# Optimization experiments

Hardware: AMD Instinct MI355X
Metric: run time of the kernel (lower is better)

## Reference

```python
import jax, jax.numpy as jnp
import numpy as np

N_NODES = 100000
N_EDGES = 3200000
IN_FEATS = 512
HIDDEN = 16
OUT_FEATS = 128
N_CLASSES = 3


def _glorot(key, shape):
    fan_in, fan_out = shape[0], shape[1]
    limit = float(np.sqrt(6.0 / (fan_in + fan_out)))
    return jax.random.uniform(key, shape, jnp.float32, -limit, limit)


def setup_inputs() -> dict:
    key = jax.random.key(0)
    ks = jax.random.split(key, 9)
    features = jax.random.normal(ks[0], (N_NODES, IN_FEATS), jnp.float32)
    src = jax.random.randint(ks[1], (N_EDGES,), 0, N_NODES, jnp.int64)
    dst = jax.random.randint(ks[2], (N_EDGES,), 0, N_NODES, jnp.int64)
    W1 = _glorot(ks[3], (IN_FEATS, HIDDEN))
    b1 = jnp.zeros((HIDDEN,), jnp.float32)
    W2 = _glorot(ks[4], (HIDDEN, OUT_FEATS))
    b2 = jnp.zeros((OUT_FEATS,), jnp.float32)
    lim = float(1.0 / np.sqrt(OUT_FEATS))
    Wfc = jax.random.uniform(ks[5], (OUT_FEATS, N_CLASSES), jnp.float32, -lim, lim)
    bfc = jax.random.uniform(ks[6], (N_CLASSES,), jnp.float32, -lim, lim)
    return {"features": features, "src": src, "dst": dst,
            "W1": W1, "b1": b1, "W2": W2, "b2": b2, "Wfc": Wfc, "bfc": bfc}


def _graph_conv(feat, src, dst, W, b):
    # DGL GraphConv, norm='both': D_out^{-1/2} A D_in^{-1/2} feat W + b
    ones = jnp.ones((src.shape[0],), feat.dtype)
    deg_out = jax.ops.segment_sum(ones, src, num_segments=N_NODES)
    deg_in = jax.ops.segment_sum(ones, dst, num_segments=N_NODES)
    norm_src = jax.lax.rsqrt(jnp.maximum(deg_out, 1.0))  # [N]
    norm_dst = jax.lax.rsqrt(jnp.maximum(deg_in, 1.0))   # [N]
    # project first (in >= out here), then aggregate over edges
    h = (feat * norm_src[:, None]) @ W                   # [N, out]
    agg = jax.ops.segment_sum(h[src], dst, num_segments=N_NODES)  # [N, out]
    return agg * norm_dst[:, None] + b


def reference(features, src, dst, W1, b1, W2, b2, Wfc, bfc):
    x = jax.nn.relu(_graph_conv(features, src, dst, W1, b1))
    x = _graph_conv(x, src, dst, W2, b2)
    return x @ Wfc + bfc
```

## Files before the change

### kernel.cpp

```cpp
#include <hip/hip_runtime.h>

#define N_NODES 100000
#define N_EDGES 3200000
#define F_IN 512
#define NH 16
#define F_OUT 128
#define NCLS 3

#define NB 782
#define BCAP 4736
#define CHUNK 4096

typedef float  f32x4 __attribute__((ext_vector_type(4)));
typedef short  s16x8 __attribute__((ext_vector_type(8)));

static __device__ __forceinline__ short f2bf(float f) {
    union { float f; unsigned u; } v; v.f = f;
    unsigned r = v.u + 0x7FFFu + ((v.u >> 16) & 1u);
    return (short)(r >> 16);
}

__global__ __launch_bounds__(256) void bin_scatter_kernel(const int* __restrict__ src,
                                                          const int* __restrict__ dst,
                                                          int* __restrict__ deg_out,
                                                          int* __restrict__ gcursor,
                                                          int* __restrict__ pairbuf) {
    __shared__ int hist[NB];
    __shared__ int base[NB];
    int t = threadIdx.x;
    for (int i = t; i < NB; i += 256) hist[i] = 0;
    __syncthreads();
    int e0 = blockIdx.x * CHUNK;
    int nE = N_EDGES - e0; if (nE > CHUNK) nE = CHUNK;
    int pk[16], bk[16], rk[16];
#pragma unroll
    for (int it = 0; it < 16; ++it) {
        int i = t + it * 256;
        bool valid = i < nE;
        int s = valid ? src[e0 + i] : 0;
        int d = valid ? dst[e0 + i] : 0;
        if (valid) atomicAdd(&deg_out[s], 1);
        int b = d >> 7;
        pk[it] = s | ((d & 127) << 17);
        bk[it] = b;
        rk[it] = valid ? atomicAdd(&hist[b], 1) : 0;
    }
    __syncthreads();
    int rot = blockIdx.x % NB;
    for (int j = t; j < NB; j += 256) {
        int b = j + rot; if (b >= NB) b -= NB;
        int h = hist[b];
        base[b] = (h > 0) ? atomicAdd(&gcursor[b], h) : 0;
    }
    __syncthreads();
#pragma unroll
    for (int it = 0; it < 16; ++it) {
        int i = t + it * 256;
        if (i < nE) {
            int b = bk[it];
            int pos = base[b] + rk[it];
            if (pos < BCAP) pairbuf[b * BCAP + pos] = pk[it];
        }
    }
}

__global__ __launch_bounds__(1024) void bucket_scan_kernel(const int* __restrict__ gcursor,
                                                           int* __restrict__ csr_base) {
    __shared__ int s[1024];
    int t = threadIdx.x;
    int v = 0;
    if (t < NB) { v = gcursor[t]; if (v > BCAP) v = BCAP; }
    s[t] = v;
    __syncthreads();
    for (int off = 1; off < 1024; off <<= 1) {
        int x = (t >= off) ? s[t - off] : 0;
        __syncthreads();
        s[t] += x;
        __syncthreads();
    }
    if (t < NB) csr_base[t] = s[t] - v;
}

__global__ __launch_bounds__(256) void bucket_csr_kernel(const int* __restrict__ gcursor,
                                                         const int* __restrict__ csr_base,
                                                         const int* __restrict__ pairbuf,
                                                         int* __restrict__ col,
                                                         int* __restrict__ row_ptr,
                                                         float* __restrict__ norm_dst) {
    __shared__ int hist[128];
    __shared__ int scn[128];
    int b = blockIdx.x;
    int t = threadIdx.x;
    if (t < 128) hist[t] = 0;
    __syncthreads();
    int c = gcursor[b]; if (c > BCAP) c = BCAP;
    const int* pb = pairbuf + b * BCAP;
    int pk[19], rk[19];
#pragma unroll
    for (int it = 0; it < 19; ++it) {
        int i = t + it * 256;
        bool valid = i < c;
        int v = valid ? pb[i] : 0;
        pk[it] = v;
        rk[it] = valid ? atomicAdd(&hist[v >> 17], 1) : 0;
    }
    __syncthreads();
    if (t < 128) scn[t] = hist[t];
    __syncthreads();
    for (int off = 1; off < 128; off <<= 1) {
        int x = (t >= off && t < 128) ? scn[t - off] : 0;
        __syncthreads();
        if (t < 128) scn[t] += x;
        __syncthreads();
    }
    int gbase = csr_base[b];
#pragma unroll
    for (int it = 0; it < 19; ++it) {
        int i = t + it * 256;
        if (i < c) {
            int v = pk[it];
            int node = v >> 17;
            int pos = gbase + (scn[node] - hist[node]) + rk[it];
            col[pos] = v & 0x1FFFF;
        }
    }
    int node = b * 128 + t;
    if (t < 128 && node < N_NODES) {
        row_ptr[node] = gbase + scn[t] - hist[t];
        norm_dst[node] = rsqrtf(fmaxf((float)hist[t], 1.0f));
    }
    if (b == NB - 1 && t == 0) row_ptr[N_NODES] = N_EDGES;
}

__global__ void norm_src_kernel(const int* __restrict__ deg_out, float* __restrict__ norm_src) {
    int i = blockIdx.x * blockDim.x + threadIdx.x;
    if (i < N_NODES) norm_src[i] = rsqrtf(fmaxf((float)deg_out[i], 1.0f));
}

__global__ void w1b_prep_kernel(const float* __restrict__ W1, unsigned short* __restrict__ W1B) {
    int idx = blockIdx.x * blockDim.x + threadIdx.x;
    if (idx >= 16 * 64 * 8) return;
    int kc = idx >> 9, lane = (idx >> 3) & 63, i = idx & 7;
    int k = kc * 32 + (lane >> 4) * 8 + i;
    int j = lane & 15;
    W1B[idx] = (unsigned short)f2bf(W1[k * NH + j]);
}

__global__ void wc_prep_kernel(const float* __restrict__ W2, const float* __restrict__ b2,
                               const float* __restrict__ Wfc, const float* __restrict__ bfc,
                               float* __restrict__ Wc) {
    int t = threadIdx.x;
    if (t < NH * NCLS) {
        int j = t / NCLS, c = t % NCLS;
        float acc = 0.0f;
        for (int k = 0; k < F_OUT; ++k) acc += W2[j * F_OUT + k] * Wfc[k * NCLS + c];
        Wc[t] = acc;
    } else if (t < NH * NCLS + NCLS) {
        int c = t - NH * NCLS;
        float acc = bfc[c];
        for (int k = 0; k < F_OUT; ++k) acc += b2[k] * Wfc[k * NCLS + c];
        Wc[t] = acc;
    }
}

__global__ __launch_bounds__(256) void gemm1_kernel(const float* __restrict__ feat,
                                                    const unsigned short* __restrict__ W1B,
                                                    const float* __restrict__ norm_src,
                                                    float* __restrict__ h1) {
    int t = threadIdx.x;
    int lane = t & 63;
    int m = lane & 15;
    int q = lane >> 4;
    const s16x8* wb = (const s16x8*)W1B;
    s16x8 B[16];
#pragma unroll
    for (int kc = 0; kc < 16; ++kc) B[kc] = wb[kc * 64 + lane];

    int w = blockIdx.x * 4 + (t >> 6);
    int nwaves = gridDim.x * 4;
    const int ntiles = N_NODES / 16;
    for (int tile = w; tile < ntiles; tile += nwaves) {
        f32x4 acc = {0.0f, 0.0f, 0.0f, 0.0f};
        const float* arow = feat + (size_t)(tile * 16 + m) * F_IN + q * 8;
#pragma unroll
        for (int kc = 0; kc < 16; ++kc) {
            f32x4 fa = *(const f32x4*)(arow + kc * 32);
            f32x4 fb = *(const f32x4*)(arow + kc * 32 + 4);
            s16x8 a;
            a[0] = f2bf(fa.x); a[1] = f2bf(fa.y); a[2] = f2bf(fa.z); a[3] = f2bf(fa.w);
            a[4] = f2bf(fb.x); a[5] = f2bf(fb.y); a[6] = f2bf(fb.z); a[7] = f2bf(fb.w);
            acc = __builtin_amdgcn_mfma_f32_16x16x32_bf16(a, B[kc], acc, 0, 0, 0);
        }
#pragma unroll
        for (int r = 0; r < 4; ++r) {
            int node = tile * 16 + q * 4 + r;
            h1[(size_t)node * NH + m] = acc[r] * norm_src[node];
        }
    }
}

__global__ __launch_bounds__(256) void agg1_kernel(const int* __restrict__ row_ptr,
                                                   const int* __restrict__ col,
                                                   const float* __restrict__ h1,
                                                   const float* __restrict__ norm_dst,
                                                   const float* __restrict__ norm_src,
                                                   const float* __restrict__ b1,
                                                   float* __restrict__ x1n) {
    int t = threadIdx.x;
    int lane = t & 63;
    int n = blockIdx.x * 4 + (t >> 6);
    int eo = lane >> 2, comp = lane & 3;
    int beg = row_ptr[n], end = row_ptr[n + 1];
    f32x4 acc = {0.0f, 0.0f, 0.0f, 0.0f};
    for (int e = beg + eo; e < end; e += 16) {
        int s = col[e];
        acc += *(const f32x4*)(h1 + (size_t)s * NH + comp * 4);
    }
#pragma unroll
    for (int sh = 4; sh <= 32; sh <<= 1) {
        acc.x += __shfl_xor(acc.x, sh); acc.y += __shfl_xor(acc.y, sh);
        acc.z += __shfl_xor(acc.z, sh); acc.w += __shfl_xor(acc.w, sh);
    }
    if (lane < 4) {
        float nd = norm_dst[n], ns = norm_src[n];
        f32x4 bv = ((const f32x4*)b1)[lane];
        f32x4 v = acc * nd + bv;
        v.x = fmaxf(v.x, 0.0f) * ns; v.y = fmaxf(v.y, 0.0f) * ns;
        v.z = fmaxf(v.z, 0.0f) * ns; v.w = fmaxf(v.w, 0.0f) * ns;
        ((f32x4*)(x1n + (size_t)n * NH))[lane] = v;
    }
}

__global__ __launch_bounds__(256) void agg2_kernel(const int* __restrict__ row_ptr,
                                                   const int* __restrict__ col,
                                                   const float* __restrict__ x1n,
                                                   const float* __restrict__ norm_dst,
                                                   const float* __restrict__ Wc,
                                                   float* __restrict__ out) {
    __shared__ float Wcs[NH * NCLS + NCLS];
    int t = threadIdx.x;
    if (t < NH * NCLS + NCLS) Wcs[t] = Wc[t];
    __syncthreads();
    int lane = t & 63;
    int n = blockIdx.x * 4 + (t >> 6);
    int eo = lane >> 2, comp = lane & 3;
    int beg = row_ptr[n], end = row_ptr[n + 1];
    f32x4 acc = {0.0f, 0.0f, 0.0f, 0.0f};
    for (int e = beg + eo; e < end; e += 16) {
        int s = col[e];
        acc += *(const f32x4*)(x1n + (size_t)s * NH + comp * 4);
    }
#pragma unroll
    for (int sh = 4; sh <= 32; sh <<= 1) {
        acc.x += __shfl_xor(acc.x, sh); acc.y += __shfl_xor(acc.y, sh);
        acc.z += __shfl_xor(acc.z, sh); acc.w += __shfl_xor(acc.w, sh);
    }
    float p0 = 0.0f, p1 = 0.0f, p2 = 0.0f;
    if (lane < 4) {
#pragma unroll
        for (int i = 0; i < 4; ++i) {
            float y = acc[i];
            int j = lane * 4 + i;
            p0 += y * Wcs[j * NCLS + 0];
            p1 += y * Wcs[j * NCLS + 1];
            p2 += y * Wcs[j * NCLS + 2];
        }
    }
    p0 += __shfl_xor(p0, 1); p0 += __shfl_xor(p0, 2);
    p1 += __shfl_xor(p1, 1); p1 += __shfl_xor(p1, 2);
    p2 += __shfl_xor(p2, 1); p2 += __shfl_xor(p2, 2);
    if (lane == 0) {
        float nd = norm_dst[n];
        out[(size_t)n * NCLS + 0] = nd * p0 + Wcs[NH * NCLS + 0];
        out[(size_t)n * NCLS + 1] = nd * p1 + Wcs[NH * NCLS + 1];
        out[(size_t)n * NCLS + 2] = nd * p2 + Wcs[NH * NCLS + 2];
    }
}

extern "C" void kernel_launch(void* const* d_in, const int* in_sizes, int n_in,
                              void* d_out, int out_size, void* d_ws, size_t ws_size,
                              hipStream_t stream) {
    const float* feat = (const float*)d_in[0];
    const int*   src  = (const int*)d_in[1];
    const int*   dst  = (const int*)d_in[2];
    const float* W1   = (const float*)d_in[3];
    const float* b1   = (const float*)d_in[4];
    const float* W2   = (const float*)d_in[5];
    const float* b2   = (const float*)d_in[6];
    const float* Wfc  = (const float*)d_in[7];
    const float* bfc  = (const float*)d_in[8];
    float* out = (float*)d_out;

    char* ws = (char*)d_ws;
    size_t off = 0;
    auto carve = [&](size_t bytes) {
        char* p = ws + off;
        off = (off + bytes + 255) & ~(size_t)255;
        return p;
    };
    int*   deg_out  = (int*)carve((size_t)N_NODES * 4);
    int*   gcursor  = (int*)carve((size_t)NB * 4);
    int*   csr_base = (int*)carve((size_t)NB * 4);
    int*   pairbuf  = (int*)carve((size_t)NB * BCAP * 4);
    int*   row_ptr  = (int*)carve((size_t)(N_NODES + 1) * 4);
    int*   col      = (int*)carve((size_t)N_EDGES * 4);
    float* norm_src = (float*)carve((size_t)N_NODES * 4);
    float* norm_dst = (float*)carve((size_t)N_NODES * 4);
    float* h1       = (float*)carve((size_t)N_NODES * NH * 4);
    float* x1n      = (float*)carve((size_t)N_NODES * NH * 4);
    unsigned short* W1B = (unsigned short*)carve(16 * 64 * 8 * 2);
    float* Wc       = (float*)carve((NH * NCLS + NCLS) * 4);
    (void)ws_size;

    hipMemsetAsync(deg_out, 0, (size_t)N_NODES * 4, stream);
    hipMemsetAsync(gcursor, 0, (size_t)NB * 4, stream);

    const int nBinBlocks = (N_EDGES + CHUNK - 1) / CHUNK;
    bin_scatter_kernel<<<nBinBlocks, 256, 0, stream>>>(src, dst, deg_out, gcursor, pairbuf);
    bucket_scan_kernel<<<1, 1024, 0, stream>>>(gcursor, csr_base);
    bucket_csr_kernel<<<NB, 256, 0, stream>>>(gcursor, csr_base, pairbuf, col, row_ptr, norm_dst);

    norm_src_kernel<<<(N_NODES + 255) / 256, 256, 0, stream>>>(deg_out, norm_src);

    w1b_prep_kernel<<<32, 256, 0, stream>>>(W1, W1B);
    wc_prep_kernel<<<1, 64, 0, stream>>>(W2, b2, Wfc, bfc, Wc);

    gemm1_kernel<<<625, 256, 0, stream>>>(feat, W1B, norm_src, h1);

    agg1_kernel<<<N_NODES / 4, 256, 0, stream>>>(row_ptr, col, h1, norm_dst, norm_src, b1, x1n);

    agg2_kernel<<<N_NODES / 4, 256, 0, stream>>>(row_ptr, col, x1n, norm_dst, Wc, out);
}
```

Baseline: 599.8 us.

## Replace CSR build with bucketed edge lists aggregated via LDS atomics

Removes the scan and per-bucket CSR construction kernels and aggregates each layer directly from 256-node destination buckets. Each bucket block accumulates neighbor features into shared memory with float atomics and counts in-degree on the fly, so the norm_src and norm_dst arrays and kernels go away. This drops several launches and the col/row_ptr memory traffic. In exchange it pays for heavy LDS atomic contention, makes float summation order nondeterministic, and silently drops edges if a bucket overflows its capacity.

```diff
diff --git a/kernel.cpp b/kernel.cpp
--- a/kernel.cpp
+++ b/kernel.cpp
@@ -7,9 +7,9 @@
 #define F_OUT 128
 #define NCLS 3
 
-#define NB 782
-#define BCAP 4736
-#define CHUNK 4096
+#define NB 391
+#define BCAP 9216
+#define CHUNK 16384
 
 typedef float  f32x4 __attribute__((ext_vector_type(4)));
 typedef short  s16x8 __attribute__((ext_vector_type(8)));
@@ -20,121 +20,38 @@
     return (short)(r >> 16);
 }
 
-__global__ __launch_bounds__(256) void bin_scatter_kernel(const int* __restrict__ src,
-                                                          const int* __restrict__ dst,
-                                                          int* __restrict__ deg_out,
-                                                          int* __restrict__ gcursor,
-                                                          int* __restrict__ pairbuf) {
+__global__ __launch_bounds__(512) void bin_kernel(const int* __restrict__ src,
+                                                  const int* __restrict__ dst,
+                                                  int* __restrict__ deg_out,
+                                                  int* __restrict__ gcursor,
+                                                  int* __restrict__ pairbuf) {
     __shared__ int hist[NB];
-    __shared__ int base[NB];
+    __shared__ int cur[NB];
     int t = threadIdx.x;
-    for (int i = t; i < NB; i += 256) hist[i] = 0;
+    for (int i = t; i < NB; i += 512) hist[i] = 0;
     __syncthreads();
     int e0 = blockIdx.x * CHUNK;
     int nE = N_EDGES - e0; if (nE > CHUNK) nE = CHUNK;
-    int pk[16], bk[16], rk[16];
-#pragma unroll
-    for (int it = 0; it < 16; ++it) {
-        int i = t + it * 256;
-        bool valid = i < nE;
-        int s = valid ? src[e0 + i] : 0;
-        int d = valid ? dst[e0 + i] : 0;
-        if (valid) atomicAdd(&deg_out[s], 1);
-        int b = d >> 7;
-        pk[it] = s | ((d & 127) << 17);
-        bk[it] = b;
-        rk[it] = valid ? atomicAdd(&hist[b], 1) : 0;
+    for (int i = t; i < nE; i += 512) {
+        int d = dst[e0 + i];
+        atomicAdd(&hist[d >> 8], 1);
     }
     __syncthreads();
     int rot = blockIdx.x % NB;
-    for (int j = t; j < NB; j += 256) {
+    for (int j = t; j < NB; j += 512) {
         int b = j + rot; if (b >= NB) b -= NB;
         int h = hist[b];
-        base[b] = (h > 0) ? atomicAdd(&gcursor[b], h) : 0;
-    }
-    __syncthreads();
-#pragma unroll
-    for (int it = 0; it < 16; ++it) {
-        int i = t + it * 256;
-        if (i < nE) {
-            int b = bk[it];
-            int pos = base[b] + rk[it];
-            if (pos < BCAP) pairbuf[b * BCAP + pos] = pk[it];
-        }
-    }
-}
-
-__global__ __launch_bounds__(1024) void bucket_scan_kernel(const int* __restrict__ gcursor,
-                                                           int* __restrict__ csr_base) {
-    __shared__ int s[1024];
-    int t = threadIdx.x;
-    int v = 0;
-    if (t < NB) { v = gcursor[t]; if (v > BCAP) v = BCAP; }
-    s[t] = v;
-    __syncthreads();
-    for (int off = 1; off < 1024; off <<= 1) {
-        int x = (t >= off) ? s[t - off] : 0;
-        __syncthreads();
-        s[t] += x;
-        __syncthreads();
-    }
-    if (t < NB) csr_base[t] = s[t] - v;
-}
-
-__global__ __launch_bounds__(256) void bucket_csr_kernel(const int* __restrict__ gcursor,
-                                                         const int* __restrict__ csr_base,
-                                                         const int* __restrict__ pairbuf,
-                                                         int* __restrict__ col,
-                                                         int* __restrict__ row_ptr,
-                                                         float* __restrict__ norm_dst) {
-    __shared__ int hist[128];
-    __shared__ int scn[128];
-    int b = blockIdx.x;
-    int t = threadIdx.x;
-    if (t < 128) hist[t] = 0;
-    __syncthreads();
-    int c = gcursor[b]; if (c > BCAP) c = BCAP;
-    const int* pb = pairbuf + b * BCAP;
-    int pk[19], rk[19];
-#pragma unroll
-    for (int it = 0; it < 19; ++it) {
-        int i = t + it * 256;
-        bool valid = i < c;
-        int v = valid ? pb[i] : 0;
-        pk[it] = v;
-        rk[it] = valid ? atomicAdd(&hist[v >> 17], 1) : 0;
-    }
-    __syncthreads();
-    if (t < 128) scn[t] = hist[t];
-    __syncthreads();
-    for (int off = 1; off < 128; off <<= 1) {
-        int x = (t >= off && t < 128) ? scn[t - off] : 0;
-        __syncthreads();
-        if (t < 128) scn[t] += x;
-        __syncthreads();
-    }
-    int gbase = csr_base[b];
-#pragma unroll
-    for (int it = 0; it < 19; ++it) {
-        int i = t + it * 256;
-        if (i < c) {
-            int v = pk[it];
-            int node = v >> 17;
-            int pos = gbase + (scn[node] - hist[node]) + rk[it];
-            col[pos] = v & 0x1FFFF;
-        }
-    }
-    int node = b * 128 + t;
-    if (t < 128 && node < N_NODES) {
-        row_ptr[node] = gbase + scn[t] - hist[t];
-        norm_dst[node] = rsqrtf(fmaxf((float)hist[t], 1.0f));
-    }
-    if (b == NB - 1 && t == 0) row_ptr[N_NODES] = N_EDGES;
-}
-
-__global__ void norm_src_kernel(const int* __restrict__ deg_out, float* __restrict__ norm_src) {
-    int i = blockIdx.x * blockDim.x + threadIdx.x;
-    if (i < N_NODES) norm_src[i] = rsqrtf(fmaxf((float)deg_out[i], 1.0f));
+        cur[b] = (h > 0) ? atomicAdd(&gcursor[b], h) : 0;
+    }
+    __syncthreads();
+    for (int i = t; i < nE; i += 512) {
+        int s = src[e0 + i];
+        int d = dst[e0 + i];
+        atomicAdd(&deg_out[s], 1);
+        int b = d >> 8;
+        int pos = atomicAdd(&cur[b], 1);
+        if (pos < BCAP) pairbuf[b * BCAP + pos] = s | ((d & 255) << 17);
+    }
 }
 
 __global__ void w1b_prep_kernel(const float* __restrict__ W1, unsigned short* __restrict__ W1B) {
@@ -165,7 +82,7 @@
 
 __global__ __launch_bounds__(256) void gemm1_kernel(const float* __restrict__ feat,
                                                     const unsigned short* __restrict__ W1B,
-                                                    const float* __restrict__ norm_src,
+                                                    const int* __restrict__ deg_out,
                                                     float* __restrict__ h1) {
     int t = threadIdx.x;
     int lane = t & 63;
@@ -194,86 +111,110 @@
 #pragma unroll
         for (int r = 0; r < 4; ++r) {
             int node = tile * 16 + q * 4 + r;
-            h1[(size_t)node * NH + m] = acc[r] * norm_src[node];
-        }
-    }
-}
-
-__global__ __launch_bounds__(256) void agg1_kernel(const int* __restrict__ row_ptr,
-                                                   const int* __restrict__ col,
-                                                   const float* __restrict__ h1,
-                                                   const float* __restrict__ norm_dst,
-                                                   const float* __restrict__ norm_src,
-                                                   const float* __restrict__ b1,
-                                                   float* __restrict__ x1n) {
-    int t = threadIdx.x;
-    int lane = t & 63;
-    int n = blockIdx.x * 4 + (t >> 6);
+            float ns = rsqrtf(fmaxf((float)deg_out[node], 1.0f));
+            h1[(size_t)node * NH + m] = acc[r] * ns;
+        }
+    }
+}
+
+__global__ __launch_bounds__(512) void agg1_bucket_kernel(const int* __restrict__ gcursor,
+                                                          const int* __restrict__ pairbuf,
+                                                          const float* __restrict__ h1,
+                                                          const int* __restrict__ deg_out,
+                                                          const float* __restrict__ b1,
+                                                          float* __restrict__ x1n) {
+    __shared__ float acc[256 * 17];
+    __shared__ int   cnt[256];
+    __shared__ float b1s[16];
+    int b = blockIdx.x, t = threadIdx.x;
+    for (int i = t; i < 256 * 17; i += 512) acc[i] = 0.0f;
+    if (t < 256) cnt[t] = 0;
+    if (t < 16) b1s[t] = b1[t];
+    __syncthreads();
+    int c = gcursor[b]; if (c > BCAP) c = BCAP;
+    const int* pb = pairbuf + (size_t)b * BCAP;
+    int lane = t & 63, w = t >> 6;
     int eo = lane >> 2, comp = lane & 3;
-    int beg = row_ptr[n], end = row_ptr[n + 1];
-    f32x4 acc = {0.0f, 0.0f, 0.0f, 0.0f};
-    for (int e = beg + eo; e < end; e += 16) {
-        int s = col[e];
-        acc += *(const f32x4*)(h1 + (size_t)s * NH + comp * 4);
-    }
-#pragma unroll
-    for (int sh = 4; sh <= 32; sh <<= 1) {
-        acc.x += __shfl_xor(acc.x, sh); acc.y += __shfl_xor(acc.y, sh);
-        acc.z += __shfl_xor(acc.z, sh); acc.w += __shfl_xor(acc.w, sh);
-    }
-    if (lane < 4) {
-        float nd = norm_dst[n], ns = norm_src[n];
-        f32x4 bv = ((const f32x4*)b1)[lane];
-        f32x4 v = acc * nd + bv;
-        v.x = fmaxf(v.x, 0.0f) * ns; v.y = fmaxf(v.y, 0.0f) * ns;
-        v.z = fmaxf(v.z, 0.0f) * ns; v.w = fmaxf(v.w, 0.0f) * ns;
-        ((f32x4*)(x1n + (size_t)n * NH))[lane] = v;
-    }
-}
-
-__global__ __launch_bounds__(256) void agg2_kernel(const int* __restrict__ row_ptr,
-                                                   const int* __restrict__ col,
-                                                   const float* __restrict__ x1n,
-                                                   const float* __restrict__ norm_dst,
-                                                   const float* __restrict__ Wc,
-                                                   float* __restrict__ out) {
+    for (int e0 = w * 16; e0 < c; e0 += 128) {
+        int e = e0 + eo;
+        if (e < c) {
+            int pk = pb[e];
+            int s = pk & 0x1FFFF;
+            int loc = pk >> 17;
+            f32x4 hv = *(const f32x4*)(h1 + (size_t)s * NH + comp * 4);
+            int base = loc * 17 + comp * 4;
+            atomicAdd(&acc[base + 0], hv.x);
+            atomicAdd(&acc[base + 1], hv.y);
+            atomicAdd(&acc[base + 2], hv.z);
+            atomicAdd(&acc[base + 3], hv.w);
+            if (comp == 0) atomicAdd(&cnt[loc], 1);
+        }
+    }
+    __syncthreads();
+    int node = b * 256 + t;
+    if (t < 256 && node < N_NODES) {
+        float nd = rsqrtf(fmaxf((float)cnt[t], 1.0f));
+        float ns = rsqrtf(fmaxf((float)deg_out[node], 1.0f));
+        f32x4* dstp = (f32x4*)(x1n + (size_t)node * NH);
+#pragma unroll
+        for (int g = 0; g < 4; ++g) {
+            f32x4 v;
+            v.x = fmaxf(acc[t * 17 + g * 4 + 0] * nd + b1s[g * 4 + 0], 0.0f) * ns;
+            v.y = fmaxf(acc[t * 17 + g * 4 + 1] * nd + b1s[g * 4 + 1], 0.0f) * ns;
+            v.z = fmaxf(acc[t * 17 + g * 4 + 2] * nd + b1s[g * 4 + 2], 0.0f) * ns;
+            v.w = fmaxf(acc[t * 17 + g * 4 + 3] * nd + b1s[g * 4 + 3], 0.0f) * ns;
+            dstp[g] = v;
+        }
+    }
+}
+
+__global__ __launch_bounds__(512) void agg2_bucket_kernel(const int* __restrict__ gcursor,
+                                                          const int* __restrict__ pairbuf,
+                                                          const float* __restrict__ x1n,
+                                                          const float* __restrict__ Wc,
+                                                          float* __restrict__ out) {
+    __shared__ float acc[256 * 17];
+    __shared__ int   cnt[256];
     __shared__ float Wcs[NH * NCLS + NCLS];
-    int t = threadIdx.x;
+    int b = blockIdx.x, t = threadIdx.x;
+    for (int i = t; i < 256 * 17; i += 512) acc[i] = 0.0f;
+    if (t < 256) cnt[t] = 0;
     if (t < NH * NCLS + NCLS) Wcs[t] = Wc[t];
     __syncthreads();
-    int lane = t & 63;
-    int n = blockIdx.x * 4 + (t >> 6);
+    int c = gcursor[b]; if (c > BCAP) c = BCAP;
+    const int* pb = pairbuf + (size_t)b * BCAP;
+    int lane = t & 63, w = t >> 6;
     int eo = lane >> 2, comp = lane & 3;
-    int beg = row_ptr[n], end = row_ptr[n + 1];
-    f32x4 acc = {0.0f, 0.0f, 0.0f, 0.0f};
-    for (int e = beg + eo; e < end; e += 16) {
-        int s = col[e];
-        acc += *(const f32x4*)(x1n + (size_t)s * NH + comp * 4);
-    }
-#pragma unroll
-    for (int sh = 4; sh <= 32; sh <<= 1) {
-        acc.x += __shfl_xor(acc.x, sh); acc.y += __shfl_xor(acc.y, sh);
-        acc.z += __shfl_xor(acc.z, sh); acc.w += __shfl_xor(acc.w, sh);
-    }
-    float p0 = 0.0f, p1 = 0.0f, p2 = 0.0f;
-    if (lane < 4) {
-#pragma unroll
-        for (int i = 0; i < 4; ++i) {
-            float y = acc[i];
-            int j = lane * 4 + i;
+    for (int e0 = w * 16; e0 < c; e0 += 128) {
+        int e = e0 + eo;
+        if (e < c) {
+            int pk = pb[e];
+            int s = pk & 0x1FFFF;
+            int loc = pk >> 17;
+            f32x4 hv = *(const f32x4*)(x1n + (size_t)s * NH + comp * 4);
+            int base = loc * 17 + comp * 4;
+            atomicAdd(&acc[base + 0], hv.x);
+            atomicAdd(&acc[base + 1], hv.y);
+            atomicAdd(&acc[base + 2], hv.z);
+            atomicAdd(&acc[base + 3], hv.w);
+            if (comp == 0) atomicAdd(&cnt[loc], 1);
+        }
+    }
+    __syncthreads();
+    int node = b * 256 + t;
+    if (t < 256 && node < N_NODES) {
+        float nd = rsqrtf(fmaxf((float)cnt[t], 1.0f));
+        float p0 = 0.0f, p1 = 0.0f, p2 = 0.0f;
+#pragma unroll
+        for (int j = 0; j < NH; ++j) {
+            float y = acc[t * 17 + j];
             p0 += y * Wcs[j * NCLS + 0];
             p1 += y * Wcs[j * NCLS + 1];
             p2 += y * Wcs[j * NCLS + 2];
         }
-    }
-    p0 += __shfl_xor(p0, 1); p0 += __shfl_xor(p0, 2);
-    p1 += __shfl_xor(p1, 1); p1 += __shfl_xor(p1, 2);
-    p2 += __shfl_xor(p2, 1); p2 += __shfl_xor(p2, 2);
-    if (lane == 0) {
-        float nd = norm_dst[n];
-        out[(size_t)n * NCLS + 0] = nd * p0 + Wcs[NH * NCLS + 0];
-        out[(size_t)n * NCLS + 1] = nd * p1 + Wcs[NH * NCLS + 1];
-        out[(size_t)n * NCLS + 2] = nd * p2 + Wcs[NH * NCLS + 2];
+        out[(size_t)node * NCLS + 0] = nd * p0 + Wcs[NH * NCLS + 0];
+        out[(size_t)node * NCLS + 1] = nd * p1 + Wcs[NH * NCLS + 1];
+        out[(size_t)node * NCLS + 2] = nd * p2 + Wcs[NH * NCLS + 2];
     }
 }
 
@@ -300,12 +241,7 @@
     };
     int*   deg_out  = (int*)carve((size_t)N_NODES * 4);
     int*   gcursor  = (int*)carve((size_t)NB * 4);
-    int*   csr_base = (int*)carve((size_t)NB * 4);
     int*   pairbuf  = (int*)carve((size_t)NB * BCAP * 4);
-    int*   row_ptr  = (int*)carve((size_t)(N_NODES + 1) * 4);
-    int*   col      = (int*)carve((size_t)N_EDGES * 4);
-    float* norm_src = (float*)carve((size_t)N_NODES * 4);
-    float* norm_dst = (float*)carve((size_t)N_NODES * 4);
     float* h1       = (float*)carve((size_t)N_NODES * NH * 4);
     float* x1n      = (float*)carve((size_t)N_NODES * NH * 4);
     unsigned short* W1B = (unsigned short*)carve(16 * 64 * 8 * 2);
@@ -316,18 +252,14 @@
     hipMemsetAsync(gcursor, 0, (size_t)NB * 4, stream);
 
     const int nBinBlocks = (N_EDGES + CHUNK - 1) / CHUNK;
-    bin_scatter_kernel<<<nBinBlocks, 256, 0, stream>>>(src, dst, deg_out, gcursor, pairbuf);
-    bucket_scan_kernel<<<1, 1024, 0, stream>>>(gcursor, csr_base);
-    bucket_csr_kernel<<<NB, 256, 0, stream>>>(gcursor, csr_base, pairbuf, col, row_ptr, norm_dst);
-
-    norm_src_kernel<<<(N_NODES + 255) / 256, 256, 0, stream>>>(deg_out, norm_src);
+    bin_kernel<<<nBinBlocks, 512, 0, stream>>>(src, dst, deg_out, gcursor, pairbuf);
 
     w1b_prep_kernel<<<32, 256, 0, stream>>>(W1, W1B);
     wc_prep_kernel<<<1, 64, 0, stream>>>(W2, b2, Wfc, bfc, Wc);
 
-    gemm1_kernel<<<625, 256, 0, stream>>>(feat, W1B, norm_src, h1);
-
-    agg1_kernel<<<N_NODES / 4, 256, 0, stream>>>(row_ptr, col, h1, norm_dst, norm_src, b1, x1n);
-
-    agg2_kernel<<<N_NODES / 4, 256, 0, stream>>>(row_ptr, col, x1n, norm_dst, Wc, out);
-}
+    gemm1_kernel<<<1250, 256, 0, stream>>>(feat, W1B, deg_out, h1);
+
+    agg1_bucket_kernel<<<NB, 512, 0, stream>>>(gcursor, pairbuf, h1, deg_out, b1, x1n);
+
+    agg2_bucket_kernel<<<NB, 512, 0, stream>>>(gcursor, pairbuf, x1n, Wc, out);
+}
```

After: 1.164 ms. 94.1% more time.
